# Kernel optimization log

Hardware: AMD Instinct MI355X
Metric: run time of the kernel (lower is better)

## Reference

```python
import jax, jax.numpy as jnp
import numpy as np

N_SRC, N_DST, N_EDGE, D_IN, D_HID, D_OUT = 100000, 25000, 300000, 256, 256, 256


def setup_inputs() -> dict:
    key = jax.random.key(0)
    ks = jax.random.split(key, 9)
    # forward tensor args
    h_src = jax.random.normal(ks[0], (N_SRC, D_IN), dtype=jnp.float32)
    h_dst = jax.random.normal(ks[1], (N_DST, D_IN), dtype=jnp.float32)
    weights = jax.random.uniform(ks[2], (N_EDGE,), dtype=jnp.float32)
    src_idx = jax.random.randint(ks[3], (N_EDGE,), 0, N_SRC)
    dst_idx = jax.random.randint(ks[4], (N_EDGE,), 0, N_DST)
    # learned parameters (xavier_uniform with relu gain, zero bias)
    gain = float(np.sqrt(2.0))
    def xavier(k, fan_in, fan_out):
        a = gain * np.sqrt(6.0 / (fan_in + fan_out))
        return jax.random.uniform(k, (fan_in, fan_out), dtype=jnp.float32, minval=-a, maxval=a)
    Q_w = xavier(ks[5], D_IN, D_HID)            # stored [in, out]
    Q_b = jnp.zeros((D_HID,), dtype=jnp.float32)
    W_w = xavier(ks[6], D_IN + D_HID, D_OUT)    # stored [in, out]
    W_b = jnp.zeros((D_OUT,), dtype=jnp.float32)
    return {"h_src": h_src, "h_dst": h_dst, "weights": weights,
            "Q_w": Q_w, "Q_b": Q_b, "W_w": W_w, "W_b": W_b,
            "src_idx": src_idx, "dst_idx": dst_idx}


def reference(h_src, h_dst, weights, Q_w, Q_b, W_w, W_b, src_idx, dst_idx):
    n_dst = h_dst.shape[0]
    # nft = relu(Q(h_src))  (dropout is eval-mode identity)
    nft = jax.nn.relu(h_src @ Q_w + Q_b)                     # [N_src, H]
    # weighted neighbor sum: u_mul_e + sum over edges per dst node
    msg = nft[src_idx] * weights[:, None]                    # [E, H]
    n = jax.ops.segment_sum(msg, dst_idx, num_segments=n_dst)          # [N_dst, H]
    ws = jax.ops.segment_sum(weights, dst_idx, num_segments=n_dst)     # [N_dst]
    ws = jnp.clip(ws, 1.0, None)[:, None]
    z = jax.nn.relu(jnp.concatenate([n / ws, h_dst], axis=1) @ W_w + W_b)  # [N_dst, O]
    z_norm = jnp.linalg.norm(z, ord=2, axis=1, keepdims=True)
    z_norm = jnp.where(z_norm == 0, jnp.float32(1.0), z_norm)
    return z / z_norm
```

## Files before the change

### kernel.cpp

```cpp
#include <hip/hip_runtime.h>
#include <hip/hip_bf16.h>
#include <cstdint>

#define N_SRC 100000
#define N_DST 25000
#define N_EDGE 300000

typedef float f32x4 __attribute__((ext_vector_type(4)));
typedef __bf16 bf16x8 __attribute__((ext_vector_type(8)));

__device__ __forceinline__ unsigned short f2bf(float f) {
    union { float f; unsigned int u; } v; v.f = f;
    unsigned int u = v.u;
    u += 0x7FFFu + ((u >> 16) & 1u);
    return (unsigned short)(u >> 16);
}
__device__ __forceinline__ float bf2f(unsigned int bits16) {
    union { unsigned int u; float f; } v; v.u = bits16 << 16;
    return v.f;
}

__global__ void cast_weights(const float* __restrict__ Qw, const float* __restrict__ Ww,
                             unsigned short* __restrict__ Qt, unsigned short* __restrict__ Wt) {
    int i = blockIdx.x * blockDim.x + threadIdx.x;
    if (i < 256 * 256) {
        int n = i >> 8, k = i & 255;
        Qt[n * 256 + k] = f2bf(Qw[k * 256 + n]);
    } else if (i < 256 * 256 + 512 * 256) {
        int j = i - 256 * 256;
        int n = j >> 9, k = j & 511;
        Wt[n * 512 + k] = f2bf(Ww[k * 256 + n]);
    }
}

__global__ void hist_kernel(const int* __restrict__ dst_idx, int* __restrict__ counts) {
    int i = blockIdx.x * blockDim.x + threadIdx.x;
    if (i < N_EDGE) atomicAdd(&counts[dst_idx[i]], 1);
}

__global__ __launch_bounds__(1024) void scan_kernel(const int* __restrict__ counts,
                                                    int* __restrict__ offsets, int n) {
    __shared__ int wsum[16];
    const int t = threadIdx.x;
    const int wid = t >> 6, lane = t & 63;
    int carry = 0;
    if (t == 0) offsets[0] = 0;
    for (int base = 0; base < n; base += 1024) {
        int x = (base + t < n) ? counts[base + t] : 0;
        #pragma unroll
        for (int off = 1; off < 64; off <<= 1) {
            int y = __shfl_up(x, off, 64);
            if (lane >= off) x += y;
        }
        if (lane == 63) wsum[wid] = x;
        __syncthreads();
        if (t < 16) {
            int w = wsum[t];
            #pragma unroll
            for (int off = 1; off < 16; off <<= 1) {
                int y = __shfl_up(w, off, 64);
                if (t >= off) w += y;
            }
            wsum[t] = w;
        }
        __syncthreads();
        int pre = (wid > 0) ? wsum[wid - 1] : 0;
        int incl = carry + pre + x;
        if (base + t < n) offsets[base + t + 1] = incl;
        carry += wsum[15];
        __syncthreads();
    }
}

__global__ void scatter_kernel(const int* __restrict__ dst_idx, const int* __restrict__ offsets,
                               int* __restrict__ counts, int* __restrict__ edge_list) {
    int i = blockIdx.x * blockDim.x + threadIdx.x;
    if (i < N_EDGE) {
        int d = dst_idx[i];
        int pos = offsets[d] + (atomicSub(&counts[d], 1) - 1);
        edge_list[pos] = i;
    }
}

template<int KDIM, bool A_BF16, bool NORM>
__global__ __launch_bounds__(256, 2) void gemm_fused(
    const float* __restrict__ Af, const unsigned short* __restrict__ Ab,
    const unsigned short* __restrict__ Bt, const float* __restrict__ bias,
    unsigned short* __restrict__ Cb, float* __restrict__ Cf, int M)
{
    constexpr int NKT = KDIM / 64;
    __shared__ __align__(16) unsigned short As[2][64 * 72];
    __shared__ float norml[4][64];

    const int tid = threadIdx.x;
    const int wave = tid >> 6, lane = tid & 63;
    const int g = lane >> 4, c = lane & 15;
    const int wn0 = wave * 64;
    const int m0 = blockIdx.x * 64;

    f32x4 acc[4][4];
    #pragma unroll
    for (int i = 0; i < 4; ++i)
        #pragma unroll
        for (int j = 0; j < 4; ++j)
            acc[i][j] = (f32x4){0.f, 0.f, 0.f, 0.f};

    float4 sf[4];
    uint4  sb[2];

    auto issueA = [&](int kt) {
        const int k0 = kt * 64;
        if constexpr (A_BF16) {
            #pragma unroll
            for (int i = 0; i < 2; ++i) {
                int idx = tid + i * 256;
                int row = idx >> 3, ch = idx & 7;
                int gm = min(m0 + row, M - 1);
                sb[i] = *reinterpret_cast<const uint4*>(Ab + (size_t)gm * KDIM + k0 + ch * 8);
            }
        } else {
            #pragma unroll
            for (int i = 0; i < 4; ++i) {
                int idx = tid + i * 256;
                int row = idx >> 4, c4 = idx & 15;
                int gm = min(m0 + row, M - 1);
                sf[i] = *reinterpret_cast<const float4*>(Af + (size_t)gm * KDIM + k0 + c4 * 4);
            }
        }
    };
    auto writeA = [&](int buf) {
        if constexpr (A_BF16) {
            #pragma unroll
            for (int i = 0; i < 2; ++i) {
                int idx = tid + i * 256;
                int row = idx >> 3, ch = idx & 7;
                *reinterpret_cast<uint4*>(&As[buf][row * 72 + ch * 8]) = sb[i];
            }
        } else {
            #pragma unroll
            for (int i = 0; i < 4; ++i) {
                int idx = tid + i * 256;
                int row = idx >> 4, c4 = idx & 15;
                uint2 p;
                p.x = (unsigned)f2bf(sf[i].x) | ((unsigned)f2bf(sf[i].y) << 16);
                p.y = (unsigned)f2bf(sf[i].z) | ((unsigned)f2bf(sf[i].w) << 16);
                *reinterpret_cast<uint2*>(&As[buf][row * 72 + c4 * 4]) = p;
            }
        }
    };

    issueA(0);
    writeA(0);
    __syncthreads();

    #pragma unroll
    for (int kt = 0; kt < NKT; ++kt) {
        const int cur = kt & 1;
        if (kt + 1 < NKT) issueA(kt + 1);
        const int k0 = kt * 64;
        bf16x8 bfrag[2][4];
        #pragma unroll
        for (int ks = 0; ks < 2; ++ks)
            #pragma unroll
            for (int ni = 0; ni < 4; ++ni)
                bfrag[ks][ni] = *reinterpret_cast<const bf16x8*>(
                    Bt + (size_t)(wn0 + ni * 16 + c) * KDIM + k0 + ks * 32 + g * 8);
        #pragma unroll
        for (int ks = 0; ks < 2; ++ks) {
            const int koff = ks * 32 + g * 8;
            bf16x8 a[4];
            #pragma unroll
            for (int mi = 0; mi < 4; ++mi)
                a[mi] = *reinterpret_cast<const bf16x8*>(&As[cur][(mi * 16 + c) * 72 + koff]);
            #pragma unroll
            for (int mi = 0; mi < 4; ++mi)
                #pragma unroll
                for (int ni = 0; ni < 4; ++ni)
                    acc[mi][ni] = __builtin_amdgcn_mfma_f32_16x16x32_bf16(a[mi], bfrag[ks][ni], acc[mi][ni], 0, 0, 0);
        }
        if (kt + 1 < NKT) writeA(cur ^ 1);
        __syncthreads();
    }

    float bcol[4];
    #pragma unroll
    for (int ni = 0; ni < 4; ++ni) bcol[ni] = bias[wn0 + ni * 16 + c];

    if constexpr (!NORM) {
        #pragma unroll
        for (int mi = 0; mi < 4; ++mi) {
            int rowb = m0 + mi * 16 + g * 4;
            #pragma unroll
            for (int ni = 0; ni < 4; ++ni) {
                int col = wn0 + ni * 16 + c;
                #pragma unroll
                for (int r = 0; r < 4; ++r) {
                    int row = rowb + r;
                    if (row < M) {
                        float v = fmaxf(acc[mi][ni][r] + bcol[ni], 0.f);
                        Cb[(size_t)row * 256 + col] = f2bf(v);
                    }
                }
            }
        }
    } else {
        float ssq[4][4];
        #pragma unroll
        for (int mi = 0; mi < 4; ++mi) {
            #pragma unroll
            for (int r = 0; r < 4; ++r) {
                float s = 0.f;
                #pragma unroll
                for (int ni = 0; ni < 4; ++ni) {
                    float v = fmaxf(acc[mi][ni][r] + bcol[ni], 0.f);
                    acc[mi][ni][r] = v;
                    s += v * v;
                }
                #pragma unroll
                for (int m = 1; m < 16; m <<= 1) s += __shfl_xor(s, m, 64);
                ssq[mi][r] = s;
            }
        }
        if (c == 0) {
            #pragma unroll
            for (int mi = 0; mi < 4; ++mi)
                #pragma unroll
                for (int r = 0; r < 4; ++r)
                    norml[wave][mi * 16 + g * 4 + r] = ssq[mi][r];
        }
        __syncthreads();
        #pragma unroll
        for (int mi = 0; mi < 4; ++mi) {
            int rowb = m0 + mi * 16 + g * 4;
            #pragma unroll
            for (int r = 0; r < 4; ++r) {
                int rl = mi * 16 + g * 4 + r;
                float tot = norml[0][rl] + norml[1][rl] + norml[2][rl] + norml[3][rl];
                float rn = tot > 0.f ? rsqrtf(tot) : 1.0f;
                int row = rowb + r;
                if (row < M) {
                    #pragma unroll
                    for (int ni = 0; ni < 4; ++ni) {
                        int col = wn0 + ni * 16 + c;
                        Cf[(size_t)row * 256 + col] = acc[mi][ni][r] * rn;
                    }
                }
            }
        }
    }
}

__global__ __launch_bounds__(256) void aggregate_kernel(
    const unsigned short* __restrict__ nft, const float* __restrict__ h_dst,
    const float* __restrict__ weights, const int* __restrict__ src_idx,
    const int* __restrict__ edge_list, const int* __restrict__ offsets,
    unsigned short* __restrict__ xb)
{
    int d = blockIdx.x * 4 + (threadIdx.x >> 6);
    if (d >= N_DST) return;
    int lane = threadIdx.x & 63;
    int p0 = offsets[d], p1 = offsets[d + 1];
    float a0 = 0.f, a1 = 0.f, a2 = 0.f, a3 = 0.f, wsum = 0.f;
    int p = p0;
    for (; p + 1 < p1; p += 2) {
        int e0 = edge_list[p], e1 = edge_list[p + 1];
        float w0 = weights[e0], w1 = weights[e1];
        int s0 = src_idx[e0], s1 = src_idx[e1];
        uint2 v0 = *reinterpret_cast<const uint2*>(nft + (size_t)s0 * 256 + lane * 4);
        uint2 v1 = *reinterpret_cast<const uint2*>(nft + (size_t)s1 * 256 + lane * 4);
        wsum += w0 + w1;
        a0 += w0 * bf2f(v0.x & 0xffffu) + w1 * bf2f(v1.x & 0xffffu);
        a1 += w0 * bf2f(v0.x >> 16)     + w1 * bf2f(v1.x >> 16);
        a2 += w0 * bf2f(v0.y & 0xffffu) + w1 * bf2f(v1.y & 0xffffu);
        a3 += w0 * bf2f(v0.y >> 16)     + w1 * bf2f(v1.y >> 16);
    }
    if (p < p1) {
        int e = edge_list[p];
        float w = weights[e];
        int s = src_idx[e];
        wsum += w;
        uint2 v = *reinterpret_cast<const uint2*>(nft + (size_t)s * 256 + lane * 4);
        a0 += w * bf2f(v.x & 0xffffu);
        a1 += w * bf2f(v.x >> 16);
        a2 += w * bf2f(v.y & 0xffffu);
        a3 += w * bf2f(v.y >> 16);
    }
    float inv = 1.0f / fmaxf(wsum, 1.0f);
    uint2 pk;
    pk.x = (unsigned)f2bf(a0 * inv) | ((unsigned)f2bf(a1 * inv) << 16);
    pk.y = (unsigned)f2bf(a2 * inv) | ((unsigned)f2bf(a3 * inv) << 16);
    *reinterpret_cast<uint2*>(xb + (size_t)d * 512 + lane * 4) = pk;
    float4 h = *reinterpret_cast<const float4*>(h_dst + (size_t)d * 256 + lane * 4);
    uint2 q;
    q.x = (unsigned)f2bf(h.x) | ((unsigned)f2bf(h.y) << 16);
    q.y = (unsigned)f2bf(h.z) | ((unsigned)f2bf(h.w) << 16);
    *reinterpret_cast<uint2*>(xb + (size_t)d * 512 + 256 + lane * 4) = q;
}

extern "C" void kernel_launch(void* const* d_in, const int* in_sizes, int n_in,
                              void* d_out, int out_size, void* d_ws, size_t ws_size,
                              hipStream_t stream) {
    const float* h_src   = (const float*)d_in[0];
    const float* h_dst   = (const float*)d_in[1];
    const float* weights = (const float*)d_in[2];
    const float* Q_w     = (const float*)d_in[3];
    const float* Q_b     = (const float*)d_in[4];
    const float* W_w     = (const float*)d_in[5];
    const float* W_b     = (const float*)d_in[6];
    const int* src_idx   = (const int*)d_in[7];
    const int* dst_idx   = (const int*)d_in[8];
    float* out = (float*)d_out;

    char* ws = (char*)d_ws;
    unsigned short* nft = (unsigned short*)(ws);
    unsigned short* xb  = (unsigned short*)(ws + 51200000);
    unsigned short* Qt  = (unsigned short*)(ws + 76800000);
    unsigned short* Wt  = (unsigned short*)(ws + 76931072);
    int* counts    = (int*)(ws + 77193216);
    int* offsets   = (int*)(ws + 77293216);
    int* edge_list = (int*)(ws + 77393220);

    hipMemsetAsync(counts, 0, N_DST * sizeof(int), stream);

    cast_weights<<<768, 256, 0, stream>>>(Q_w, W_w, Qt, Wt);
    hist_kernel<<<(N_EDGE + 255) / 256, 256, 0, stream>>>(dst_idx, counts);
    scan_kernel<<<1, 1024, 0, stream>>>(counts, offsets, N_DST);
    scatter_kernel<<<(N_EDGE + 255) / 256, 256, 0, stream>>>(dst_idx, offsets, counts, edge_list);

    gemm_fused<256, false, false><<<(N_SRC + 63) / 64, 256, 0, stream>>>(
        h_src, nullptr, Qt, Q_b, nft, nullptr, N_SRC);

    aggregate_kernel<<<N_DST / 4, 256, 0, stream>>>(
        nft, h_dst, weights, src_idx, edge_list, offsets, xb);

    gemm_fused<512, true, true><<<(N_DST + 63) / 64, 256, 0, stream>>>(
        nullptr, xb, Wt, W_b, nullptr, out, N_DST);

    (void)in_sizes; (void)n_in; (void)out_size; (void)ws_size;
}
```

Before: 188.8 us.

## Rewrite GEMMs with direct-to-LDS async loads and a four-stage software pipeline

Replaces the register-staged double-buffered A-tile loads with global_load_lds direct-to-LDS transfers into a 4-deep ring of XOR-swizzled buffers. The schedule is hand-unrolled with explicit vmcnt waits and raw barriers, so several stages stay in flight while MFMAs run. B fragments are now prefetched into registers in chunks with inline asm loads. For the fp32 A path, the bf16 conversion moves from the staging step to after the LDS read. The aim is to hide global memory latency and drop the VGPR round-trip, at the cost of fragile manual waitcnt bookkeeping and higher register pressure from holding B in registers.

```diff
diff --git a/kernel.cpp b/kernel.cpp
--- a/kernel.cpp
+++ b/kernel.cpp
@@ -8,6 +8,9 @@
 
 typedef float f32x4 __attribute__((ext_vector_type(4)));
 typedef __bf16 bf16x8 __attribute__((ext_vector_type(8)));
+
+typedef const __attribute__((address_space(1))) void gv_t;
+typedef __attribute__((address_space(3))) void lv_t;
 
 __device__ __forceinline__ unsigned short f2bf(float f) {
     union { float f; unsigned int u; } v; v.f = f;
@@ -19,6 +22,14 @@
     union { unsigned int u; float f; } v; v.u = bits16 << 16;
     return v.f;
 }
+
+__device__ __forceinline__ void gload16(uint4& d, const void* p) {
+    asm volatile("global_load_dwordx4 %0, %1, off" : "=v"(d) : "v"(p) : "memory");
+}
+
+#define VMWAIT(N) do { asm volatile("s_waitcnt vmcnt(" #N ")" ::: "memory"); \
+                       __builtin_amdgcn_sched_barrier(0); } while (0)
+#define BAR() __builtin_amdgcn_s_barrier()
 
 __global__ void cast_weights(const float* __restrict__ Qw, const float* __restrict__ Ww,
                              unsigned short* __restrict__ Qt, unsigned short* __restrict__ Wt) {
@@ -82,22 +93,22 @@
     }
 }
 
-template<int KDIM, bool A_BF16, bool NORM>
-__global__ __launch_bounds__(256, 2) void gemm_fused(
+template<int KDIM, bool A_F32, bool NORM>
+__global__ __launch_bounds__(256, 2) void gemm_pipe(
     const float* __restrict__ Af, const unsigned short* __restrict__ Ab,
     const unsigned short* __restrict__ Bt, const float* __restrict__ bias,
     unsigned short* __restrict__ Cb, float* __restrict__ Cf, int M)
 {
-    constexpr int NKT = KDIM / 64;
-    __shared__ __align__(16) unsigned short As[2][64 * 72];
+    __shared__ __align__(16) unsigned char Abuf[4][8192];
     __shared__ float norml[4][64];
 
     const int tid = threadIdx.x;
-    const int wave = tid >> 6, lane = tid & 63;
-    const int g = lane >> 4, c = lane & 15;
-    const int wn0 = wave * 64;
+    const int wv = tid >> 6, lane = tid & 63;
+    const int g = lane >> 4, cl = lane & 15;
     const int m0 = blockIdx.x * 64;
-
+    const int bn0 = wv * 64;
+
+    uint4 bU[4][4];
     f32x4 acc[4][4];
     #pragma unroll
     for (int i = 0; i < 4; ++i)
@@ -105,86 +116,89 @@
         for (int j = 0; j < 4; ++j)
             acc[i][j] = (f32x4){0.f, 0.f, 0.f, 0.f};
 
-    float4 sf[4];
-    uint4  sb[2];
-
-    auto issueA = [&](int kt) {
-        const int k0 = kt * 64;
-        if constexpr (A_BF16) {
-            #pragma unroll
-            for (int i = 0; i < 2; ++i) {
-                int idx = tid + i * 256;
-                int row = idx >> 3, ch = idx & 7;
-                int gm = min(m0 + row, M - 1);
-                sb[i] = *reinterpret_cast<const uint4*>(Ab + (size_t)gm * KDIM + k0 + ch * 8);
-            }
-        } else {
-            #pragma unroll
-            for (int i = 0; i < 4; ++i) {
-                int idx = tid + i * 256;
-                int row = idx >> 4, c4 = idx & 15;
-                int gm = min(m0 + row, M - 1);
-                sf[i] = *reinterpret_cast<const float4*>(Af + (size_t)gm * KDIM + k0 + c4 * 4);
-            }
-        }
-    };
-    auto writeA = [&](int buf) {
-        if constexpr (A_BF16) {
-            #pragma unroll
-            for (int i = 0; i < 2; ++i) {
-                int idx = tid + i * 256;
-                int row = idx >> 3, ch = idx & 7;
-                *reinterpret_cast<uint4*>(&As[buf][row * 72 + ch * 8]) = sb[i];
-            }
-        } else {
-            #pragma unroll
-            for (int i = 0; i < 4; ++i) {
-                int idx = tid + i * 256;
-                int row = idx >> 4, c4 = idx & 15;
-                uint2 p;
-                p.x = (unsigned)f2bf(sf[i].x) | ((unsigned)f2bf(sf[i].y) << 16);
-                p.y = (unsigned)f2bf(sf[i].z) | ((unsigned)f2bf(sf[i].w) << 16);
-                *reinterpret_cast<uint2*>(&As[buf][row * 72 + c4 * 4]) = p;
-            }
-        }
-    };
-
-    issueA(0);
-    writeA(0);
-    __syncthreads();
-
-    #pragma unroll
-    for (int kt = 0; kt < NKT; ++kt) {
-        const int cur = kt & 1;
-        if (kt + 1 < NKT) issueA(kt + 1);
-        const int k0 = kt * 64;
-        bf16x8 bfrag[2][4];
-        #pragma unroll
-        for (int ks = 0; ks < 2; ++ks)
-            #pragma unroll
-            for (int ni = 0; ni < 4; ++ni)
-                bfrag[ks][ni] = *reinterpret_cast<const bf16x8*>(
-                    Bt + (size_t)(wn0 + ni * 16 + c) * KDIM + k0 + ks * 32 + g * 8);
-        #pragma unroll
-        for (int ks = 0; ks < 2; ++ks) {
-            const int koff = ks * 32 + g * 8;
-            bf16x8 a[4];
-            #pragma unroll
-            for (int mi = 0; mi < 4; ++mi)
-                a[mi] = *reinterpret_cast<const bf16x8*>(&As[cur][(mi * 16 + c) * 72 + koff]);
-            #pragma unroll
-            for (int mi = 0; mi < 4; ++mi)
-                #pragma unroll
-                for (int ni = 0; ni < 4; ++ni)
-                    acc[mi][ni] = __builtin_amdgcn_mfma_f32_16x16x32_bf16(a[mi], bfrag[ks][ni], acc[mi][ni], 0, 0, 0);
-        }
-        if (kt + 1 < NKT) writeA(cur ^ 1);
-        __syncthreads();
-    }
+#define BLOAD(cch) do { \
+    _Pragma("unroll") \
+    for (int ni = 0; ni < 4; ++ni) { \
+        _Pragma("unroll") \
+        for (int q = 0; q < 4; ++q) \
+            gload16(bU[ni][q], Bt + (size_t)(bn0 + ni * 16 + cl) * KDIM + ((cch) * 4 + q) * 32 + g * 8); \
+    } } while (0)
+
+#define STAGE(t) do { \
+    _Pragma("unroll") \
+    for (int j = 0; j < 2; ++j) { \
+        const int chunk = wv * 2 + j; \
+        const int row = chunk * 8 + (lane >> 3); \
+        int grow = m0 + row; if (grow > M - 1) grow = M - 1; \
+        const int sws = (lane & 7) ^ (row & 7); \
+        if constexpr (A_F32) { \
+            const float* gp = Af + (size_t)grow * KDIM + (t) * 32 + sws * 4; \
+            __builtin_amdgcn_global_load_lds((gv_t*)gp, (lv_t*)&Abuf[(t) & 3][chunk * 1024], 16, 0, 0); \
+        } else { \
+            const unsigned short* gp = Ab + (size_t)grow * KDIM + (t) * 64 + sws * 8; \
+            __builtin_amdgcn_global_load_lds((gv_t*)gp, (lv_t*)&Abuf[(t) & 3][chunk * 1024], 16, 0, 0); \
+        } \
+    } } while (0)
+
+#define COMPUTE(t) do { \
+    if constexpr (A_F32) { \
+        _Pragma("unroll") \
+        for (int mi = 0; mi < 4; ++mi) { \
+            const int row = mi * 16 + cl; \
+            const f32x4 lo = *(const f32x4*)&Abuf[(t) & 3][row * 128 + ((g * 2 + 0) ^ (cl & 7)) * 16]; \
+            const f32x4 hi = *(const f32x4*)&Abuf[(t) & 3][row * 128 + ((g * 2 + 1) ^ (cl & 7)) * 16]; \
+            bf16x8 af; \
+            af[0] = (__bf16)lo[0]; af[1] = (__bf16)lo[1]; af[2] = (__bf16)lo[2]; af[3] = (__bf16)lo[3]; \
+            af[4] = (__bf16)hi[0]; af[5] = (__bf16)hi[1]; af[6] = (__bf16)hi[2]; af[7] = (__bf16)hi[3]; \
+            _Pragma("unroll") \
+            for (int ni = 0; ni < 4; ++ni) \
+                acc[mi][ni] = __builtin_amdgcn_mfma_f32_16x16x32_bf16( \
+                    af, __builtin_bit_cast(bf16x8, bU[ni][(t) & 3]), acc[mi][ni], 0, 0, 0); \
+        } \
+    } else { \
+        _Pragma("unroll") \
+        for (int ks = 0; ks < 2; ++ks) { \
+            _Pragma("unroll") \
+            for (int mi = 0; mi < 4; ++mi) { \
+                const int row = mi * 16 + cl; \
+                const bf16x8 af = *(const bf16x8*)&Abuf[(t) & 3][row * 128 + (((ks) * 4 + g) ^ (cl & 7)) * 16]; \
+                _Pragma("unroll") \
+                for (int ni = 0; ni < 4; ++ni) \
+                    acc[mi][ni] = __builtin_amdgcn_mfma_f32_16x16x32_bf16( \
+                        af, __builtin_bit_cast(bf16x8, bU[ni][((t) * 2 + (ks)) & 3]), acc[mi][ni], 0, 0, 0); \
+            } \
+        } \
+    } } while (0)
+
+    BLOAD(0);
+    STAGE(0); STAGE(1); STAGE(2);
+
+    VMWAIT(4); BAR();
+    STAGE(3); COMPUTE(0);
+    VMWAIT(4); BAR();
+    STAGE(4); COMPUTE(1);
+    if constexpr (A_F32) {
+        VMWAIT(4); BAR(); STAGE(5); COMPUTE(2);
+        VMWAIT(4); BAR(); STAGE(6); COMPUTE(3);
+        VMWAIT(4); BAR(); BLOAD(1); STAGE(7); VMWAIT(2); COMPUTE(4);
+        BAR(); COMPUTE(5);
+        BAR(); COMPUTE(6);
+        VMWAIT(0); BAR(); COMPUTE(7);
+    } else {
+        VMWAIT(4); BAR(); BLOAD(1); STAGE(5); VMWAIT(2); COMPUTE(2);
+        BAR(); STAGE(6); COMPUTE(3);
+        VMWAIT(4); BAR(); BLOAD(2); STAGE(7); VMWAIT(2); COMPUTE(4);
+        BAR(); COMPUTE(5);
+        BAR(); BLOAD(3); VMWAIT(0); COMPUTE(6);
+        BAR(); COMPUTE(7);
+    }
+#undef BLOAD
+#undef STAGE
+#undef COMPUTE
 
     float bcol[4];
     #pragma unroll
-    for (int ni = 0; ni < 4; ++ni) bcol[ni] = bias[wn0 + ni * 16 + c];
+    for (int ni = 0; ni < 4; ++ni) bcol[ni] = bias[bn0 + ni * 16 + cl];
 
     if constexpr (!NORM) {
         #pragma unroll
@@ -192,7 +206,7 @@
             int rowb = m0 + mi * 16 + g * 4;
             #pragma unroll
             for (int ni = 0; ni < 4; ++ni) {
-                int col = wn0 + ni * 16 + c;
+                int col = bn0 + ni * 16 + cl;
                 #pragma unroll
                 for (int r = 0; r < 4; ++r) {
                     int row = rowb + r;
@@ -221,12 +235,13 @@
                 ssq[mi][r] = s;
             }
         }
-        if (c == 0) {
+        __syncthreads();
+        if (cl == 0) {
             #pragma unroll
             for (int mi = 0; mi < 4; ++mi)
                 #pragma unroll
                 for (int r = 0; r < 4; ++r)
-                    norml[wave][mi * 16 + g * 4 + r] = ssq[mi][r];
+                    norml[wv][mi * 16 + g * 4 + r] = ssq[mi][r];
         }
         __syncthreads();
         #pragma unroll
@@ -241,7 +256,7 @@
                 if (row < M) {
                     #pragma unroll
                     for (int ni = 0; ni < 4; ++ni) {
-                        int col = wn0 + ni * 16 + c;
+                        int col = bn0 + ni * 16 + cl;
                         Cf[(size_t)row * 256 + col] = acc[mi][ni][r] * rn;
                     }
                 }
@@ -327,13 +342,13 @@
     scan_kernel<<<1, 1024, 0, stream>>>(counts, offsets, N_DST);
     scatter_kernel<<<(N_EDGE + 255) / 256, 256, 0, stream>>>(dst_idx, offsets, counts, edge_list);
 
-    gemm_fused<256, false, false><<<(N_SRC + 63) / 64, 256, 0, stream>>>(
+    gemm_pipe<256, true, false><<<(N_SRC + 63) / 64, 256, 0, stream>>>(
         h_src, nullptr, Qt, Q_b, nft, nullptr, N_SRC);
 
     aggregate_kernel<<<N_DST / 4, 256, 0, stream>>>(
         nft, h_dst, weights, src_idx, edge_list, offsets, xb);
 
-    gemm_fused<512, true, true><<<(N_DST + 63) / 64, 256, 0, stream>>>(
+    gemm_pipe<512, false, true><<<(N_DST + 63) / 64, 256, 0, stream>>>(
         nullptr, xb, Wt, W_b, nullptr, out, N_DST);
 
     (void)in_sizes; (void)n_in; (void)out_size; (void)ws_size;
```

New measurement: 199.5 us. 1.06x slower.

## Replace shared-memory GEMMs with per-wave register-direct 32x128 MFMA tiles

Applied to the files above, without the earlier changes.

Both GEMMs drop the LDS-staged A tile and block-wide barriers. Each wave now computes a 32x128 output tile, loading A fragments straight from global memory into registers with a three-slot prefetch ring and converting fp32 to bf16 in registers for the first GEMM. The second GEMM pairs two waves per row tile and combines their partial squared norms through a small shared array. Removing LDS traffic and per-k-step syncs trades away cross-wave A reuse, so each wave loads A and B itself, which increases global and L2 traffic and register pressure.

```diff
diff --git a/kernel.cpp b/kernel.cpp
--- a/kernel.cpp
+++ b/kernel.cpp
@@ -82,169 +82,167 @@
     }
 }
 
-template<int KDIM, bool A_BF16, bool NORM>
-__global__ __launch_bounds__(256, 2) void gemm_fused(
-    const float* __restrict__ Af, const unsigned short* __restrict__ Ab,
-    const unsigned short* __restrict__ Bt, const float* __restrict__ bias,
-    unsigned short* __restrict__ Cb, float* __restrict__ Cf, int M)
+__global__ __launch_bounds__(256, 3) void gemm1_wave(
+    const float* __restrict__ Af, const unsigned short* __restrict__ Bt,
+    const float* __restrict__ bias, unsigned short* __restrict__ Cb)
 {
-    constexpr int NKT = KDIM / 64;
-    __shared__ __align__(16) unsigned short As[2][64 * 72];
-    __shared__ float norml[4][64];
-
-    const int tid = threadIdx.x;
-    const int wave = tid >> 6, lane = tid & 63;
-    const int g = lane >> 4, c = lane & 15;
-    const int wn0 = wave * 64;
-    const int m0 = blockIdx.x * 64;
-
-    f32x4 acc[4][4];
-    #pragma unroll
-    for (int i = 0; i < 4; ++i)
-        #pragma unroll
-        for (int j = 0; j < 4; ++j)
-            acc[i][j] = (f32x4){0.f, 0.f, 0.f, 0.f};
-
-    float4 sf[4];
-    uint4  sb[2];
-
-    auto issueA = [&](int kt) {
-        const int k0 = kt * 64;
-        if constexpr (A_BF16) {
-            #pragma unroll
-            for (int i = 0; i < 2; ++i) {
-                int idx = tid + i * 256;
-                int row = idx >> 3, ch = idx & 7;
-                int gm = min(m0 + row, M - 1);
-                sb[i] = *reinterpret_cast<const uint4*>(Ab + (size_t)gm * KDIM + k0 + ch * 8);
+    const int gw = blockIdx.x * 4 + (threadIdx.x >> 6);
+    const int mt = gw >> 1, nt = gw & 1;
+    if (mt >= 3125) return;
+    const int lane = threadIdx.x & 63, g = lane >> 4, cl = lane & 15;
+    const int m0 = mt * 32, n0 = nt * 128;
+
+    f32x4 acc[2][8];
+    #pragma unroll
+    for (int mi = 0; mi < 2; ++mi)
+        #pragma unroll
+        for (int ni = 0; ni < 8; ++ni)
+            acc[mi][ni] = (f32x4){0.f, 0.f, 0.f, 0.f};
+
+    float4 Ar[3][2][2];
+    uint4  Br[8];
+
+    auto loadA = [&](int slot, int kt) {
+        #pragma unroll
+        for (int mi = 0; mi < 2; ++mi) {
+            const float* p = Af + (size_t)(m0 + mi * 16 + cl) * 256 + kt * 32 + g * 8;
+            Ar[slot][mi][0] = *reinterpret_cast<const float4*>(p);
+            Ar[slot][mi][1] = *reinterpret_cast<const float4*>(p + 4);
+        }
+    };
+    loadA(0, 0);
+    loadA(1, 1);
+
+    #pragma unroll
+    for (int kt = 0; kt < 8; ++kt) {
+        #pragma unroll
+        for (int ni = 0; ni < 8; ++ni)
+            Br[ni] = *reinterpret_cast<const uint4*>(
+                Bt + (size_t)(n0 + ni * 16 + cl) * 256 + kt * 32 + g * 8);
+        if (kt + 2 < 8) loadA((kt + 2) % 3, kt + 2);
+        #pragma unroll
+        for (int mi = 0; mi < 2; ++mi) {
+            const float4 lo = Ar[kt % 3][mi][0];
+            const float4 hi = Ar[kt % 3][mi][1];
+            bf16x8 af;
+            af[0] = (__bf16)lo.x; af[1] = (__bf16)lo.y; af[2] = (__bf16)lo.z; af[3] = (__bf16)lo.w;
+            af[4] = (__bf16)hi.x; af[5] = (__bf16)hi.y; af[6] = (__bf16)hi.z; af[7] = (__bf16)hi.w;
+            #pragma unroll
+            for (int ni = 0; ni < 8; ++ni)
+                acc[mi][ni] = __builtin_amdgcn_mfma_f32_16x16x32_bf16(
+                    af, __builtin_bit_cast(bf16x8, Br[ni]), acc[mi][ni], 0, 0, 0);
+        }
+    }
+
+    float bcol[8];
+    #pragma unroll
+    for (int ni = 0; ni < 8; ++ni) bcol[ni] = bias[n0 + ni * 16 + cl];
+
+    #pragma unroll
+    for (int mi = 0; mi < 2; ++mi) {
+        const int rowb = m0 + mi * 16 + g * 4;
+        #pragma unroll
+        for (int ni = 0; ni < 8; ++ni) {
+            const int col = n0 + ni * 16 + cl;
+            #pragma unroll
+            for (int r = 0; r < 4; ++r) {
+                float v = fmaxf(acc[mi][ni][r] + bcol[ni], 0.f);
+                Cb[(size_t)(rowb + r) * 256 + col] = f2bf(v);
             }
-        } else {
-            #pragma unroll
-            for (int i = 0; i < 4; ++i) {
-                int idx = tid + i * 256;
-                int row = idx >> 4, c4 = idx & 15;
-                int gm = min(m0 + row, M - 1);
-                sf[i] = *reinterpret_cast<const float4*>(Af + (size_t)gm * KDIM + k0 + c4 * 4);
+        }
+    }
+}
+
+__global__ __launch_bounds__(256, 3) void gemm2_wave(
+    const unsigned short* __restrict__ Ab, const unsigned short* __restrict__ Bt,
+    const float* __restrict__ bias, float* __restrict__ Cf, int M)
+{
+    __shared__ float norml[4][32];
+    const int wv = threadIdx.x >> 6;
+    const int gw = blockIdx.x * 2 + (wv >> 1);
+    const int nt = wv & 1;
+    const int lane = threadIdx.x & 63, g = lane >> 4, cl = lane & 15;
+    const int m0 = gw * 32, n0 = nt * 128;
+
+    f32x4 acc[2][8];
+    #pragma unroll
+    for (int mi = 0; mi < 2; ++mi)
+        #pragma unroll
+        for (int ni = 0; ni < 8; ++ni)
+            acc[mi][ni] = (f32x4){0.f, 0.f, 0.f, 0.f};
+
+    uint4 Ar[3][2];
+    uint4 Br[8];
+
+    auto loadA = [&](int slot, int kt) {
+        #pragma unroll
+        for (int mi = 0; mi < 2; ++mi) {
+            int row = m0 + mi * 16 + cl; if (row > M - 1) row = M - 1;
+            Ar[slot][mi] = *reinterpret_cast<const uint4*>(
+                Ab + (size_t)row * 512 + kt * 32 + g * 8);
+        }
+    };
+    loadA(0, 0);
+    loadA(1, 1);
+
+    #pragma unroll
+    for (int kt = 0; kt < 16; ++kt) {
+        #pragma unroll
+        for (int ni = 0; ni < 8; ++ni)
+            Br[ni] = *reinterpret_cast<const uint4*>(
+                Bt + (size_t)(n0 + ni * 16 + cl) * 512 + kt * 32 + g * 8);
+        if (kt + 2 < 16) loadA((kt + 2) % 3, kt + 2);
+        #pragma unroll
+        for (int mi = 0; mi < 2; ++mi) {
+            const bf16x8 af = __builtin_bit_cast(bf16x8, Ar[kt % 3][mi]);
+            #pragma unroll
+            for (int ni = 0; ni < 8; ++ni)
+                acc[mi][ni] = __builtin_amdgcn_mfma_f32_16x16x32_bf16(
+                    af, __builtin_bit_cast(bf16x8, Br[ni]), acc[mi][ni], 0, 0, 0);
+        }
+    }
+
+    float bcol[8];
+    #pragma unroll
+    for (int ni = 0; ni < 8; ++ni) bcol[ni] = bias[n0 + ni * 16 + cl];
+
+    float ssq[2][4];
+    #pragma unroll
+    for (int mi = 0; mi < 2; ++mi) {
+        #pragma unroll
+        for (int r = 0; r < 4; ++r) {
+            float s = 0.f;
+            #pragma unroll
+            for (int ni = 0; ni < 8; ++ni) {
+                float v = fmaxf(acc[mi][ni][r] + bcol[ni], 0.f);
+                acc[mi][ni][r] = v;
+                s += v * v;
             }
-        }
-    };
-    auto writeA = [&](int buf) {
-        if constexpr (A_BF16) {
-            #pragma unroll
-            for (int i = 0; i < 2; ++i) {
-                int idx = tid + i * 256;
-                int row = idx >> 3, ch = idx & 7;
-                *reinterpret_cast<uint4*>(&As[buf][row * 72 + ch * 8]) = sb[i];
-            }
-        } else {
-            #pragma unroll
-            for (int i = 0; i < 4; ++i) {
-                int idx = tid + i * 256;
-                int row = idx >> 4, c4 = idx & 15;
-                uint2 p;
-                p.x = (unsigned)f2bf(sf[i].x) | ((unsigned)f2bf(sf[i].y) << 16);
-                p.y = (unsigned)f2bf(sf[i].z) | ((unsigned)f2bf(sf[i].w) << 16);
-                *reinterpret_cast<uint2*>(&As[buf][row * 72 + c4 * 4]) = p;
-            }
-        }
-    };
-
-    issueA(0);
-    writeA(0);
+            #pragma unroll
+            for (int m = 1; m < 16; m <<= 1) s += __shfl_xor(s, m, 64);
+            ssq[mi][r] = s;
+        }
+    }
+    if (cl == 0) {
+        #pragma unroll
+        for (int mi = 0; mi < 2; ++mi)
+            #pragma unroll
+            for (int r = 0; r < 4; ++r)
+                norml[wv][mi * 16 + g * 4 + r] = ssq[mi][r];
+    }
     __syncthreads();
-
-    #pragma unroll
-    for (int kt = 0; kt < NKT; ++kt) {
-        const int cur = kt & 1;
-        if (kt + 1 < NKT) issueA(kt + 1);
-        const int k0 = kt * 64;
-        bf16x8 bfrag[2][4];
-        #pragma unroll
-        for (int ks = 0; ks < 2; ++ks)
-            #pragma unroll
-            for (int ni = 0; ni < 4; ++ni)
-                bfrag[ks][ni] = *reinterpret_cast<const bf16x8*>(
-                    Bt + (size_t)(wn0 + ni * 16 + c) * KDIM + k0 + ks * 32 + g * 8);
-        #pragma unroll
-        for (int ks = 0; ks < 2; ++ks) {
-            const int koff = ks * 32 + g * 8;
-            bf16x8 a[4];
-            #pragma unroll
-            for (int mi = 0; mi < 4; ++mi)
-                a[mi] = *reinterpret_cast<const bf16x8*>(&As[cur][(mi * 16 + c) * 72 + koff]);
-            #pragma unroll
-            for (int mi = 0; mi < 4; ++mi)
+    #pragma unroll
+    for (int mi = 0; mi < 2; ++mi) {
+        #pragma unroll
+        for (int r = 0; r < 4; ++r) {
+            const int rl = mi * 16 + g * 4 + r;
+            const float tot = norml[wv][rl] + norml[wv ^ 1][rl];
+            const float rn = tot > 0.f ? rsqrtf(tot) : 1.0f;
+            const int row = m0 + rl;
+            if (row < M) {
                 #pragma unroll
-                for (int ni = 0; ni < 4; ++ni)
-                    acc[mi][ni] = __builtin_amdgcn_mfma_f32_16x16x32_bf16(a[mi], bfrag[ks][ni], acc[mi][ni], 0, 0, 0);
-        }
-        if (kt + 1 < NKT) writeA(cur ^ 1);
-        __syncthreads();
-    }
-
-    float bcol[4];
-    #pragma unroll
-    for (int ni = 0; ni < 4; ++ni) bcol[ni] = bias[wn0 + ni * 16 + c];
-
-    if constexpr (!NORM) {
-        #pragma unroll
-        for (int mi = 0; mi < 4; ++mi) {
-            int rowb = m0 + mi * 16 + g * 4;
-            #pragma unroll
-            for (int ni = 0; ni < 4; ++ni) {
-                int col = wn0 + ni * 16 + c;
-                #pragma unroll
-                for (int r = 0; r < 4; ++r) {
-                    int row = rowb + r;
-                    if (row < M) {
-                        float v = fmaxf(acc[mi][ni][r] + bcol[ni], 0.f);
-                        Cb[(size_t)row * 256 + col] = f2bf(v);
-                    }
-                }
-            }
-        }
-    } else {
-        float ssq[4][4];
-        #pragma unroll
-        for (int mi = 0; mi < 4; ++mi) {
-            #pragma unroll
-            for (int r = 0; r < 4; ++r) {
-                float s = 0.f;
-                #pragma unroll
-                for (int ni = 0; ni < 4; ++ni) {
-                    float v = fmaxf(acc[mi][ni][r] + bcol[ni], 0.f);
-                    acc[mi][ni][r] = v;
-                    s += v * v;
-                }
-                #pragma unroll
-                for (int m = 1; m < 16; m <<= 1) s += __shfl_xor(s, m, 64);
-                ssq[mi][r] = s;
-            }
-        }
-        if (c == 0) {
-            #pragma unroll
-            for (int mi = 0; mi < 4; ++mi)
-                #pragma unroll
-                for (int r = 0; r < 4; ++r)
-                    norml[wave][mi * 16 + g * 4 + r] = ssq[mi][r];
-        }
-        __syncthreads();
-        #pragma unroll
-        for (int mi = 0; mi < 4; ++mi) {
-            int rowb = m0 + mi * 16 + g * 4;
-            #pragma unroll
-            for (int r = 0; r < 4; ++r) {
-                int rl = mi * 16 + g * 4 + r;
-                float tot = norml[0][rl] + norml[1][rl] + norml[2][rl] + norml[3][rl];
-                float rn = tot > 0.f ? rsqrtf(tot) : 1.0f;
-                int row = rowb + r;
-                if (row < M) {
-                    #pragma unroll
-                    for (int ni = 0; ni < 4; ++ni) {
-                        int col = wn0 + ni * 16 + c;
-                        Cf[(size_t)row * 256 + col] = acc[mi][ni][r] * rn;
-                    }
-                }
+                for (int ni = 0; ni < 8; ++ni)
+                    Cf[(size_t)row * 256 + n0 + ni * 16 + cl] = acc[mi][ni][r] * rn;
             }
         }
     }
@@ -327,14 +325,12 @@
     scan_kernel<<<1, 1024, 0, stream>>>(counts, offsets, N_DST);
     scatter_kernel<<<(N_EDGE + 255) / 256, 256, 0, stream>>>(dst_idx, offsets, counts, edge_list);
 
-    gemm_fused<256, false, false><<<(N_SRC + 63) / 64, 256, 0, stream>>>(
-        h_src, nullptr, Qt, Q_b, nft, nullptr, N_SRC);
+    gemm1_wave<<<1563, 256, 0, stream>>>(h_src, Qt, Q_b, nft);
 
     aggregate_kernel<<<N_DST / 4, 256, 0, stream>>>(
         nft, h_dst, weights, src_idx, edge_list, offsets, xb);
 
-    gemm_fused<512, true, true><<<(N_DST + 63) / 64, 256, 0, stream>>>(
-        nullptr, xb, Wt, W_b, nullptr, out, N_DST);
+    gemm2_wave<<<391, 256, 0, stream>>>(xb, Wt, W_b, out, N_DST);
 
     (void)in_sizes; (void)n_in; (void)out_size; (void)ws_size;
 }
```

After: 236.3 us. +25.2%, slower.

## Replace LDS-staged GEMM with register-pipelined direct-load wave GEMM

Applied to the files above, without the earlier changes.

Both GEMMs drop the shared-memory A tile and instead load A and B fragments straight from global memory into registers with inline-asm dwordx4 loads. A three-deep A / two-deep B register pipeline uses explicit vmcnt waits in place of block barriers. Blocks grow to 512 threads (8 waves, 2 row groups x 4 column tiles, 32x64 per wave), and the norm reduction now splits per row group. The aim is to remove LDS traffic and __syncthreads stalls and to keep more loads in flight. The cost is higher register pressure and duplicate global A loads across the column-tile waves, and correctness now depends on getting the manual waitcnt counts right.

```diff
diff --git a/kernel.cpp b/kernel.cpp
--- a/kernel.cpp
+++ b/kernel.cpp
@@ -18,6 +18,17 @@
 __device__ __forceinline__ float bf2f(unsigned int bits16) {
     union { unsigned int u; float f; } v; v.u = bits16 << 16;
     return v.f;
+}
+
+__device__ __forceinline__ void gload16(uint4& d, const void* p) {
+    asm volatile("global_load_dwordx4 %0, %1, off" : "=v"(d) : "v"(p) : "memory");
+}
+__device__ __forceinline__ void gload16(float4& d, const void* p) {
+    asm volatile("global_load_dwordx4 %0, %1, off" : "=v"(d) : "v"(p) : "memory");
+}
+template<int N> __device__ __forceinline__ void vmwait() {
+    asm volatile("s_waitcnt vmcnt(%0)" :: "n"(N) : "memory");
+    __builtin_amdgcn_sched_barrier(0);
 }
 
 __global__ void cast_weights(const float* __restrict__ Qw, const float* __restrict__ Ww,
@@ -82,120 +93,107 @@
     }
 }
 
-template<int KDIM, bool A_BF16, bool NORM>
-__global__ __launch_bounds__(256, 2) void gemm_fused(
+template<int KDIM, bool A_F32, bool NORM>
+__global__ __launch_bounds__(512, 3) void gemm_wave(
     const float* __restrict__ Af, const unsigned short* __restrict__ Ab,
     const unsigned short* __restrict__ Bt, const float* __restrict__ bias,
     unsigned short* __restrict__ Cb, float* __restrict__ Cf, int M)
 {
-    constexpr int NKT = KDIM / 64;
-    __shared__ __align__(16) unsigned short As[2][64 * 72];
-    __shared__ float norml[4][64];
+    constexpr int NKS = KDIM / 32;
+    constexpr int IA  = A_F32 ? 4 : 2;
+    __shared__ float norml[2][4][32];
 
     const int tid = threadIdx.x;
-    const int wave = tid >> 6, lane = tid & 63;
-    const int g = lane >> 4, c = lane & 15;
-    const int wn0 = wave * 64;
-    const int m0 = blockIdx.x * 64;
-
-    f32x4 acc[4][4];
+    const int wv = tid >> 6, lane = tid & 63;
+    const int rg = wv >> 2, nt = wv & 3;
+    const int g = lane >> 4, cl = lane & 15;
+    const int m0 = blockIdx.x * 64 + rg * 32;
+    const int n0 = nt * 64;
+
+    f32x4 acc[2][4];
     #pragma unroll
-    for (int i = 0; i < 4; ++i)
+    for (int i = 0; i < 2; ++i)
         #pragma unroll
         for (int j = 0; j < 4; ++j)
             acc[i][j] = (f32x4){0.f, 0.f, 0.f, 0.f};
 
-    float4 sf[4];
-    uint4  sb[2];
-
-    auto issueA = [&](int kt) {
-        const int k0 = kt * 64;
-        if constexpr (A_BF16) {
-            #pragma unroll
-            for (int i = 0; i < 2; ++i) {
-                int idx = tid + i * 256;
-                int row = idx >> 3, ch = idx & 7;
-                int gm = min(m0 + row, M - 1);
-                sb[i] = *reinterpret_cast<const uint4*>(Ab + (size_t)gm * KDIM + k0 + ch * 8);
-            }
+    const int rA0 = min(m0 + cl,      M - 1);
+    const int rA1 = min(m0 + 16 + cl, M - 1);
+
+    float4 Arf[3][2][2];
+    uint4  Arb[3][2];
+    uint4  Br[2][4];
+
+    auto issueA = [&](int slot, int s) {
+        if constexpr (A_F32) {
+            const float* p0 = Af + (size_t)rA0 * KDIM + s * 32 + g * 8;
+            const float* p1 = Af + (size_t)rA1 * KDIM + s * 32 + g * 8;
+            gload16(Arf[slot][0][0], p0); gload16(Arf[slot][0][1], p0 + 4);
+            gload16(Arf[slot][1][0], p1); gload16(Arf[slot][1][1], p1 + 4);
         } else {
-            #pragma unroll
-            for (int i = 0; i < 4; ++i) {
-                int idx = tid + i * 256;
-                int row = idx >> 4, c4 = idx & 15;
-                int gm = min(m0 + row, M - 1);
-                sf[i] = *reinterpret_cast<const float4*>(Af + (size_t)gm * KDIM + k0 + c4 * 4);
-            }
+            gload16(Arb[slot][0], Ab + (size_t)rA0 * KDIM + s * 32 + g * 8);
+            gload16(Arb[slot][1], Ab + (size_t)rA1 * KDIM + s * 32 + g * 8);
         }
     };
-    auto writeA = [&](int buf) {
-        if constexpr (A_BF16) {
-            #pragma unroll
-            for (int i = 0; i < 2; ++i) {
-                int idx = tid + i * 256;
-                int row = idx >> 3, ch = idx & 7;
-                *reinterpret_cast<uint4*>(&As[buf][row * 72 + ch * 8]) = sb[i];
+    auto issueB = [&](int slot, int s) {
+        #pragma unroll
+        for (int ni = 0; ni < 4; ++ni)
+            gload16(Br[slot][ni],
+                    Bt + (size_t)(n0 + ni * 16 + cl) * KDIM + s * 32 + g * 8);
+    };
+    auto compute = [&](int s) {
+        bf16x8 af[2];
+        if constexpr (A_F32) {
+            #pragma unroll
+            for (int mi = 0; mi < 2; ++mi) {
+                const float4 lo = Arf[s % 3][mi][0], hi = Arf[s % 3][mi][1];
+                af[mi][0] = (__bf16)lo.x; af[mi][1] = (__bf16)lo.y;
+                af[mi][2] = (__bf16)lo.z; af[mi][3] = (__bf16)lo.w;
+                af[mi][4] = (__bf16)hi.x; af[mi][5] = (__bf16)hi.y;
+                af[mi][6] = (__bf16)hi.z; af[mi][7] = (__bf16)hi.w;
             }
         } else {
-            #pragma unroll
-            for (int i = 0; i < 4; ++i) {
-                int idx = tid + i * 256;
-                int row = idx >> 4, c4 = idx & 15;
-                uint2 p;
-                p.x = (unsigned)f2bf(sf[i].x) | ((unsigned)f2bf(sf[i].y) << 16);
-                p.y = (unsigned)f2bf(sf[i].z) | ((unsigned)f2bf(sf[i].w) << 16);
-                *reinterpret_cast<uint2*>(&As[buf][row * 72 + c4 * 4]) = p;
-            }
-        }
+            af[0] = __builtin_bit_cast(bf16x8, Arb[s % 3][0]);
+            af[1] = __builtin_bit_cast(bf16x8, Arb[s % 3][1]);
+        }
+        #pragma unroll
+        for (int mi = 0; mi < 2; ++mi)
+            #pragma unroll
+            for (int ni = 0; ni < 4; ++ni)
+                acc[mi][ni] = __builtin_amdgcn_mfma_f32_16x16x32_bf16(
+                    af[mi], __builtin_bit_cast(bf16x8, Br[s & 1][ni]), acc[mi][ni], 0, 0, 0);
     };
 
-    issueA(0);
-    writeA(0);
-    __syncthreads();
-
+    issueB(0, 0); issueA(0, 0); issueA(1, 1); issueB(1, 1); issueA(2, 2);
+    vmwait<4 + 2 * IA>();
+    compute(0);
     #pragma unroll
-    for (int kt = 0; kt < NKT; ++kt) {
-        const int cur = kt & 1;
-        if (kt + 1 < NKT) issueA(kt + 1);
-        const int k0 = kt * 64;
-        bf16x8 bfrag[2][4];
-        #pragma unroll
-        for (int ks = 0; ks < 2; ++ks)
-            #pragma unroll
-            for (int ni = 0; ni < 4; ++ni)
-                bfrag[ks][ni] = *reinterpret_cast<const bf16x8*>(
-                    Bt + (size_t)(wn0 + ni * 16 + c) * KDIM + k0 + ks * 32 + g * 8);
-        #pragma unroll
-        for (int ks = 0; ks < 2; ++ks) {
-            const int koff = ks * 32 + g * 8;
-            bf16x8 a[4];
-            #pragma unroll
-            for (int mi = 0; mi < 4; ++mi)
-                a[mi] = *reinterpret_cast<const bf16x8*>(&As[cur][(mi * 16 + c) * 72 + koff]);
-            #pragma unroll
-            for (int mi = 0; mi < 4; ++mi)
-                #pragma unroll
-                for (int ni = 0; ni < 4; ++ni)
-                    acc[mi][ni] = __builtin_amdgcn_mfma_f32_16x16x32_bf16(a[mi], bfrag[ks][ni], acc[mi][ni], 0, 0, 0);
-        }
-        if (kt + 1 < NKT) writeA(cur ^ 1);
-        __syncthreads();
-    }
+    for (int s = 1; s <= NKS - 3; ++s) {
+        issueB((s + 1) & 1, s + 1);
+        issueA((s + 2) % 3, s + 2);
+        vmwait<4 + 2 * IA>();
+        compute(s);
+    }
+    issueB((NKS - 1) & 1, NKS - 1);
+    vmwait<4 + IA>();
+    compute(NKS - 2);
+    vmwait<0>();
+    compute(NKS - 1);
 
     float bcol[4];
     #pragma unroll
-    for (int ni = 0; ni < 4; ++ni) bcol[ni] = bias[wn0 + ni * 16 + c];
+    for (int ni = 0; ni < 4; ++ni) bcol[ni] = bias[n0 + ni * 16 + cl];
 
     if constexpr (!NORM) {
         #pragma unroll
-        for (int mi = 0; mi < 4; ++mi) {
-            int rowb = m0 + mi * 16 + g * 4;
+        for (int mi = 0; mi < 2; ++mi) {
+            const int rowb = m0 + mi * 16 + g * 4;
             #pragma unroll
             for (int ni = 0; ni < 4; ++ni) {
-                int col = wn0 + ni * 16 + c;
+                const int col = n0 + ni * 16 + cl;
                 #pragma unroll
                 for (int r = 0; r < 4; ++r) {
-                    int row = rowb + r;
+                    const int row = rowb + r;
                     if (row < M) {
                         float v = fmaxf(acc[mi][ni][r] + bcol[ni], 0.f);
                         Cb[(size_t)row * 256 + col] = f2bf(v);
@@ -204,9 +202,8 @@
             }
         }
     } else {
-        float ssq[4][4];
-        #pragma unroll
-        for (int mi = 0; mi < 4; ++mi) {
+        #pragma unroll
+        for (int mi = 0; mi < 2; ++mi) {
             #pragma unroll
             for (int r = 0; r < 4; ++r) {
                 float s = 0.f;
@@ -218,32 +215,23 @@
                 }
                 #pragma unroll
                 for (int m = 1; m < 16; m <<= 1) s += __shfl_xor(s, m, 64);
-                ssq[mi][r] = s;
-            }
-        }
-        if (c == 0) {
-            #pragma unroll
-            for (int mi = 0; mi < 4; ++mi)
-                #pragma unroll
-                for (int r = 0; r < 4; ++r)
-                    norml[wave][mi * 16 + g * 4 + r] = ssq[mi][r];
+                if (cl == 0) norml[rg][nt][mi * 16 + g * 4 + r] = s;
+            }
         }
         __syncthreads();
         #pragma unroll
-        for (int mi = 0; mi < 4; ++mi) {
-            int rowb = m0 + mi * 16 + g * 4;
+        for (int mi = 0; mi < 2; ++mi) {
             #pragma unroll
             for (int r = 0; r < 4; ++r) {
-                int rl = mi * 16 + g * 4 + r;
-                float tot = norml[0][rl] + norml[1][rl] + norml[2][rl] + norml[3][rl];
-                float rn = tot > 0.f ? rsqrtf(tot) : 1.0f;
-                int row = rowb + r;
+                const int rl = mi * 16 + g * 4 + r;
+                const float tot = norml[rg][0][rl] + norml[rg][1][rl]
+                                + norml[rg][2][rl] + norml[rg][3][rl];
+                const float rn = tot > 0.f ? rsqrtf(tot) : 1.0f;
+                const int row = m0 + rl;
                 if (row < M) {
                     #pragma unroll
-                    for (int ni = 0; ni < 4; ++ni) {
-                        int col = wn0 + ni * 16 + c;
-                        Cf[(size_t)row * 256 + col] = acc[mi][ni][r] * rn;
-                    }
+                    for (int ni = 0; ni < 4; ++ni)
+                        Cf[(size_t)row * 256 + n0 + ni * 16 + cl] = acc[mi][ni][r] * rn;
                 }
             }
         }
@@ -327,13 +315,13 @@
     scan_kernel<<<1, 1024, 0, stream>>>(counts, offsets, N_DST);
     scatter_kernel<<<(N_EDGE + 255) / 256, 256, 0, stream>>>(dst_idx, offsets, counts, edge_list);
 
-    gemm_fused<256, false, false><<<(N_SRC + 63) / 64, 256, 0, stream>>>(
+    gemm_wave<256, true, false><<<(N_SRC + 63) / 64, 512, 0, stream>>>(
         h_src, nullptr, Qt, Q_b, nft, nullptr, N_SRC);
 
     aggregate_kernel<<<N_DST / 4, 256, 0, stream>>>(
         nft, h_dst, weights, src_idx, edge_list, offsets, xb);
 
-    gemm_fused<512, true, true><<<(N_DST + 63) / 64, 256, 0, stream>>>(
+    gemm_wave<512, false, true><<<(N_DST + 63) / 64, 512, 0, stream>>>(
         nullptr, xb, Wt, W_b, nullptr, out, N_DST);
 
     (void)in_sizes; (void)n_in; (void)out_size; (void)ws_size;
```

New measurement: 268.7 us. +42.4%, slower.
